# Optimization experiments

Hardware: AMD Instinct MI355X
Metric: run time of the kernel (lower is better)

Reference implementation:

```python
import jax, jax.numpy as jnp
import numpy as np
import math

B, S, D, H = 4, 2048, 1024, 16
HD = D // H  # 64

def setup_inputs() -> dict:
    key = jax.random.key(0)
    ks = jax.random.split(key, 4)
    x = jax.random.normal(ks[0], (B, S, D), dtype=jnp.float32)
    # causal mask, True = attend (precomputed as in the original usage)
    mask = jnp.tril(jnp.ones((S, S), dtype=bool))[None, None, :, :]
    c_attn_w = jax.random.normal(ks[1], (D, 3 * D), dtype=jnp.float32) * 0.02
    c_attn_b = jnp.zeros((3 * D,), dtype=jnp.float32)
    c_proj_w = jax.random.normal(ks[2], (D, D), dtype=jnp.float32) * 0.02
    c_proj_b = jnp.zeros((D,), dtype=jnp.float32)
    return {"x": x, "mask": mask, "c_attn_w": c_attn_w, "c_attn_b": c_attn_b,
            "c_proj_w": c_proj_w, "c_proj_b": c_proj_b}

def reference(x, mask, c_attn_w, c_attn_b, c_proj_w, c_proj_b):
    b, s, d = x.shape
    # c_attn: Conv1D acts as Linear with transposed weight convention
    qkv = x @ c_attn_w + c_attn_b                      # [B,S,3D]
    q, k, v = jnp.split(qkv, 3, axis=-1)
    q = q.reshape(b, s, H, HD).transpose(0, 2, 1, 3)   # [B,H,S,hd]
    k = k.reshape(b, s, H, HD).transpose(0, 2, 1, 3)   # [B,H,S,hd]
    v = v.reshape(b, s, H, HD).transpose(0, 2, 1, 3)   # [B,H,S,hd]
    # scores, scale by sqrt(head_dim) (done unconditionally in _attn)
    w = jnp.einsum('bhqd,bhkd->bhqk', q, k) / math.sqrt(HD)
    # masked_fill_(1 - mask, -10000.0)
    w = jnp.where(mask, w, jnp.float32(-10000.0))
    w = jax.nn.softmax(w, axis=-1)                     # attn_dropout p=0
    a = jnp.einsum('bhqk,bhkd->bhqd', w, v)            # [B,H,S,hd]
    a = a.transpose(0, 2, 1, 3).reshape(b, s, d)       # merge heads
    out = a @ c_proj_w + c_proj_b                      # resid_dropout p=0
    return out
```

## Files before the change

kernel.cpp:

```cpp
#include <hip/hip_runtime.h>

#define SEQ  2048
#define DIM  1024
#define NH   16
#define HD   64
#define NB   4

typedef __bf16 bf16_t;
typedef bf16_t bf16x8 __attribute__((ext_vector_type(8)));
typedef bf16_t bf16x4 __attribute__((ext_vector_type(4)));
typedef float  floatx4 __attribute__((ext_vector_type(4)));

#define MFMA16(a, b, c) __builtin_amdgcn_mfma_f32_16x16x32_bf16((a), (b), (c), 0, 0, 0)

__device__ __forceinline__ void gl_lds16(const bf16_t* g, bf16_t* l) {
    __builtin_amdgcn_global_load_lds(
        (const __attribute__((address_space(1))) void*)g,
        (__attribute__((address_space(3))) void*)l,
        16, 0, 0);
}

__global__ __launch_bounds__(256) void prep(
    const float* __restrict__ x, bf16_t* __restrict__ xb,
    const float* __restrict__ wqkv, bf16_t* __restrict__ wqkvT,
    const float* __restrict__ wproj, bf16_t* __restrict__ wprojT) {
    const int bid = blockIdx.x, tid = threadIdx.x;
    if (bid < 8192) {
        const int i = (bid * 256 + tid) * 4;
        const float4 v = *(const float4*)(x + i);
        xb[i + 0] = (bf16_t)v.x;
        xb[i + 1] = (bf16_t)v.y;
        xb[i + 2] = (bf16_t)v.z;
        xb[i + 3] = (bf16_t)v.w;
        return;
    }
    __shared__ bf16_t t[32][33];
    const float* in;
    bf16_t* out;
    int R, C, bx, by;
    if (bid < 8192 + 3072) {
        const int idx = bid - 8192;
        in = wqkv; out = wqkvT; R = 1024; C = 3072;
        bx = idx % 96; by = idx / 96;
    } else {
        const int idx = bid - 11264;
        in = wproj; out = wprojT; R = 1024; C = 1024;
        bx = idx & 31; by = idx >> 5;
    }
    const int c0 = bx * 32, r0 = by * 32;
    const int tx = tid & 31, ty = tid >> 5;
#pragma unroll
    for (int i = 0; i < 32; i += 8)
        t[ty + i][tx] = (bf16_t)in[(r0 + ty + i) * C + c0 + tx];
    __syncthreads();
#pragma unroll
    for (int i = 0; i < 32; i += 8)
        out[(c0 + ty + i) * R + r0 + tx] = t[tx][ty + i];
}

template <int MODE>
__global__ __launch_bounds__(256, 2) void gemm128(
    const bf16_t* __restrict__ A, const bf16_t* __restrict__ Bt,
    const float* __restrict__ bias, int K,
    bf16_t* __restrict__ Qo, bf16_t* __restrict__ Ko, bf16_t* __restrict__ Vo,
    float* __restrict__ Co) {
    __shared__ __align__(16) bf16_t smem[MODE == 0 ? 128 * 136 : 128 * 128];
    bf16_t* Al = smem;
    bf16_t* Bl = smem + 128 * 64;

    const int tid = threadIdx.x;
    const int m0 = blockIdx.y * 128, n0 = blockIdx.x * 128;
    const int w = tid >> 6, lane = tid & 63;
    const int l15 = lane & 15, quad = lane >> 4;
    const int wm = (w & 1) * 64, wn = (w >> 1) * 64;

    floatx4 acc[4][4] = {};

    const int g_st = ((tid & 7) - (tid >> 3)) & 7;
    const bf16_t* aptr = A + (m0 + (tid >> 3)) * K + g_st * 8;
    const bf16_t* bptr = Bt + (n0 + (tid >> 3)) * K + g_st * 8;
    bf16_t* al = Al + tid * 8;
    bf16_t* bl = Bl + tid * 8;

    for (int k0 = 0; k0 < K; k0 += 64) {
#pragma unroll
        for (int c = 0; c < 4; c++) {
            gl_lds16(aptr + (c * 32) * K, al + c * 2048);
            gl_lds16(bptr + (c * 32) * K, bl + c * 2048);
        }
        aptr += 64;
        bptr += 64;
        __syncthreads();

#pragma unroll
        for (int h = 0; h < 2; h++) {
            const int sAB = (((h << 2) + quad + (l15 & 7)) & 7) * 8;
            bf16x8 af[4], bfr[4];
#pragma unroll
            for (int i = 0; i < 4; i++)
                af[i] = *(const bf16x8*)&Al[(wm + i * 16 + l15) * 64 + sAB];
#pragma unroll
            for (int j = 0; j < 4; j++)
                bfr[j] = *(const bf16x8*)&Bl[(wn + j * 16 + l15) * 64 + sAB];
#pragma unroll
            for (int i = 0; i < 4; i++)
#pragma unroll
                for (int j = 0; j < 4; j++)
                    acc[i][j] = MODE == 0 ? MFMA16(bfr[j], af[i], acc[i][j])
                                          : MFMA16(af[i], bfr[j], acc[i][j]);
        }
        __syncthreads();
    }

    if (MODE == 0) {
        bf16_t* Cl = smem;
        const int which = n0 >> 10;
        const float qs = (which == 0) ? 0.125f * 1.44269504f : 1.0f;
#pragma unroll
        for (int j = 0; j < 4; j++) {
            const int nc = wn + j * 16 + quad * 4;
#pragma unroll
            for (int i = 0; i < 4; i++) {
                const int mrow = wm + i * 16 + l15;
                bf16x4 pk;
#pragma unroll
                for (int r = 0; r < 4; r++)
                    pk[r] = (bf16_t)((acc[i][j][r] + bias[n0 + nc + r]) * qs);
                *(bf16x4*)&Cl[mrow * 136 + nc] = pk;
            }
        }
        __syncthreads();

        if (which < 2) {
            const int row = tid >> 1, ch = (tid & 1) << 6;
            const int m = m0 + row, b = m >> 11, s = m & 2047;
            const int h = ((n0 & 1023) >> 6) + (ch >> 6);
            bf16_t* dst = (which == 0 ? Qo : Ko) + ((size_t)(b * NH + h) * SEQ + s) * HD;
            const bf16_t* src = Cl + row * 136 + ch;
#pragma unroll
            for (int g = 0; g < 8; g++)
                *(bf16x8*)(dst + g * 8) = *(const bf16x8*)(src + g * 8);
        } else {
            const int dl = tid & 127, sh = (tid >> 7) << 6;
            const int h = ((n0 & 1023) >> 6) + (dl >> 6), d = dl & 63;
            const int b = m0 >> 11, sbase = (m0 & 2047) + sh;
            bf16_t* dst = Vo + ((size_t)(b * NH + h) * HD + d) * SEQ + sbase;
#pragma unroll
            for (int g = 0; g < 8; g++) {
                bf16x8 tv;
#pragma unroll
                for (int e = 0; e < 8; e++)
                    tv[e] = Cl[(sh + g * 8 + e) * 136 + dl];
                *(bf16x8*)(dst + g * 8) = tv;
            }
        }
    } else {
#pragma unroll
        for (int j = 0; j < 4; j++) {
            const int n = n0 + wn + j * 16 + l15;
            const float bv = bias[n];
#pragma unroll
            for (int i = 0; i < 4; i++)
#pragma unroll
                for (int r = 0; r < 4; r++) {
                    const int m = m0 + wm + i * 16 + quad * 4 + r;
                    Co[m * 1024 + n] = acc[i][j][r] + bv;
                }
        }
    }
}

__global__ __launch_bounds__(256, 2) void attn2q(
    const bf16_t* __restrict__ Q, const bf16_t* __restrict__ Kg,
    const bf16_t* __restrict__ Vt, bf16_t* __restrict__ Aout) {
    __shared__ bf16_t Ks[2 * 64 * 64];
    __shared__ bf16_t Vs[2 * 64 * 64];
    __shared__ bf16_t Ps[128 * 64];

    const int bh = blockIdx.y;
    const int px = (blockIdx.x + (bh >> 3)) & 7;
    const int qtA = 15 - px, qtB = px;
    const int nkA = 2 * qtA + 2, nkB = 2 * qtB + 2;

    const int tid = threadIdx.x, w = tid >> 6, lane = tid & 63;
    const int l15 = lane & 15, quad = lane >> 4;
    const int b = bh >> 4, hd = bh & 15;
    const int xk = l15 & 7;

    bf16x8 aqA[2][2], aqB[2][2];
#pragma unroll
    for (int i = 0; i < 2; i++) {
        const bf16_t* qrA = Q + (size_t)(bh * SEQ + qtA * 128 + w * 32 + i * 16 + l15) * HD;
        const bf16_t* qrB = Q + (size_t)(bh * SEQ + qtB * 128 + w * 32 + i * 16 + l15) * HD;
#pragma unroll
        for (int h = 0; h < 2; h++) {
            aqA[i][h] = *(const bf16x8*)(qrA + h * 32 + quad * 8);
            aqB[i][h] = *(const bf16x8*)(qrB + h * 32 + quad * 8);
        }
    }

    floatx4 oA[2][4] = {}, oB[2][4] = {};
    float liA[2] = {}, liB[2] = {};

    const int r_st = tid >> 2, g0 = tid & 3;
    const bf16_t* kgl = Kg + (size_t)bh * SEQ * HD + (size_t)r_st * HD;
    const bf16_t* vgl = Vt + (size_t)bh * HD * SEQ + (size_t)r_st * SEQ;
    const int sw0 = ((g0 ^ (r_st & 7)) * 8);
    const int sw1 = (((g0 + 4) ^ (r_st & 7)) * 8);

    auto proc = [&](int qt, bf16x8 (&aq)[2][2], floatx4 (&o)[2][4],
                    float (&li)[2], int kt, int sub) {
        const bf16_t* Ksub = Ks + sub * 4096;
        const bf16_t* Vsub = Vs + sub * 4096;
        bf16x8 bk[4][2];
#pragma unroll
        for (int j = 0; j < 4; j++) {
            const int n = j * 16 + l15;
#pragma unroll
            for (int h = 0; h < 2; h++)
                bk[j][h] = *(const bf16x8*)&Ksub[n * 64 + (((h * 4 + quad) ^ xk) * 8)];
        }
        floatx4 z[2][4] = {};
#pragma unroll
        for (int i = 0; i < 2; i++)
#pragma unroll
            for (int j = 0; j < 4; j++) {
                z[i][j] = MFMA16(bk[j][0], aq[i][0], z[i][j]);
                z[i][j] = MFMA16(bk[j][1], aq[i][1], z[i][j]);
            }
#pragma unroll
        for (int i = 0; i < 2; i++) {
            const int qbase = qt * 128 + w * 32 + i * 16;
            const int qrow_l = qbase + l15;
            const bool full = (kt * 64 + 63) <= qbase;
            const int prow = w * 32 + i * 16 + l15;
            bf16_t* pbase = Ps + prow * 64;
            const int rx = prow & 7;
#pragma unroll
            for (int j = 0; j < 4; j++) {
                const int kg0 = kt * 64 + j * 16 + quad * 4;
                bf16x4 pk;
#pragma unroll
                for (int r = 0; r < 4; r++) {
                    float e = __builtin_amdgcn_exp2f(z[i][j][r]);
                    if (!full && kg0 + r > qrow_l) e = 0.f;
                    li[i] += e;
                    pk[r] = (bf16_t)e;
                }
                const int g = 2 * j + (quad >> 1);
                *(bf16x4*)(pbase + (((g ^ rx) << 3) | ((quad & 1) << 2))) = pk;
            }
        }
        __builtin_amdgcn_s_waitcnt(0xC07F);
        bf16x8 ap[2][2];
#pragma unroll
        for (int i = 0; i < 2; i++) {
            const int row = w * 32 + i * 16 + l15;
#pragma unroll
            for (int kk = 0; kk < 2; kk++)
                ap[i][kk] = *(const bf16x8*)&Ps[row * 64 +
                                               (((kk * 4 + quad) ^ (row & 7)) << 3)];
        }
        bf16x8 bv[4][2];
#pragma unroll
        for (int j = 0; j < 4; j++) {
            const int n = j * 16 + l15;
#pragma unroll
            for (int kk = 0; kk < 2; kk++)
                bv[j][kk] = *(const bf16x8*)&Vsub[n * 64 + (((kk * 4 + quad) ^ xk) * 8)];
        }
#pragma unroll
        for (int i = 0; i < 2; i++)
#pragma unroll
            for (int j = 0; j < 4; j++) {
                o[i][j] = MFMA16(ap[i][0], bv[j][0], o[i][j]);
                o[i][j] = MFMA16(ap[i][1], bv[j][1], o[i][j]);
            }
    };

    for (int ktp = 0; ktp < nkA; ktp += 2) {
#pragma unroll
        for (int sub = 0; sub < 2; ++sub) {
            const int kt = ktp + sub;
            const bf16x8 k0 = *(const bf16x8*)(kgl + kt * 64 * HD + g0 * 8);
            const bf16x8 k1 = *(const bf16x8*)(kgl + kt * 64 * HD + (g0 + 4) * 8);
            const bf16x8 v0 = *(const bf16x8*)(vgl + kt * 64 + g0 * 8);
            const bf16x8 v1 = *(const bf16x8*)(vgl + kt * 64 + (g0 + 4) * 8);
            bf16_t* ks = Ks + sub * 4096 + r_st * 64;
            bf16_t* vs = Vs + sub * 4096 + r_st * 64;
            *(bf16x8*)(ks + sw0) = k0;
            *(bf16x8*)(ks + sw1) = k1;
            *(bf16x8*)(vs + sw0) = v0;
            *(bf16x8*)(vs + sw1) = v1;
        }
        __syncthreads();
#pragma unroll
        for (int sub = 0; sub < 2; ++sub) {
            const int kt = ktp + sub;
            proc(qtA, aqA, oA, liA, kt, sub);
            if (kt < nkB) proc(qtB, aqB, oB, liB, kt, sub);
        }
        __syncthreads();
    }

#pragma unroll
    for (int t = 0; t < 2; t++) {
        const int qt = t == 0 ? qtA : qtB;
        floatx4(&o)[2][4] = t == 0 ? oA : oB;
        float(&li)[2] = t == 0 ? liA : liB;
#pragma unroll
        for (int i = 0; i < 2; i++) {
            float s = li[i];
            s += __shfl_xor(s, 16, 64);
            s += __shfl_xor(s, 32, 64);
#pragma unroll
            for (int r = 0; r < 4; r++) {
                const float sv = __shfl(s, quad * 4 + r, 64);
                const float inv = 1.0f / sv;
                const int srow = qt * 128 + w * 32 + i * 16 + quad * 4 + r;
                bf16_t* orow = Aout + (size_t)(b * SEQ + srow) * DIM + hd * HD;
#pragma unroll
                for (int j = 0; j < 4; j++)
                    orow[j * 16 + l15] = (bf16_t)(o[i][j][r] * inv);
            }
        }
    }
}

extern "C" void kernel_launch(void* const* d_in, const int* in_sizes, int n_in,
                              void* d_out, int out_size, void* d_ws, size_t ws_size,
                              hipStream_t stream) {
    const float* x        = (const float*)d_in[0];
    const float* c_attn_w = (const float*)d_in[2];
    const float* c_attn_b = (const float*)d_in[3];
    const float* c_proj_w = (const float*)d_in[4];
    const float* c_proj_b = (const float*)d_in[5];
    float* out = (float*)d_out;

    char* ws = (char*)d_ws;
    bf16_t* xb     = (bf16_t*)ws; ws += (size_t)NB * SEQ * DIM * 2;
    bf16_t* wqkvT  = (bf16_t*)ws; ws += (size_t)3072 * 1024 * 2;
    bf16_t* wprojT = (bf16_t*)ws; ws += (size_t)1024 * 1024 * 2;
    bf16_t* Qb  = (bf16_t*)ws; ws += (size_t)NB * NH * SEQ * HD * 2;
    bf16_t* Kb  = (bf16_t*)ws; ws += (size_t)NB * NH * SEQ * HD * 2;
    bf16_t* Vtb = (bf16_t*)ws; ws += (size_t)NB * NH * SEQ * HD * 2;
    bf16_t* Ab  = (bf16_t*)ws; ws += (size_t)NB * SEQ * DIM * 2;

    prep<<<12288, 256, 0, stream>>>(x, xb, c_attn_w, wqkvT, c_proj_w, wprojT);

    gemm128<0><<<dim3(24, 64), 256, 0, stream>>>(xb, wqkvT, c_attn_b, 1024,
                                                 Qb, Kb, Vtb, nullptr);

    attn2q<<<dim3(8, NB * NH), 256, 0, stream>>>(Qb, Kb, Vtb, Ab);

    gemm128<1><<<dim3(8, 64), 256, 0, stream>>>(Ab, wprojT, c_proj_b, 1024,
                                                nullptr, nullptr, nullptr, out);
}
```

Baseline: 267.0 us.

## Prefetch next K/V tile pair into registers during attention compute

The attention loop now issues the global loads for the next pair of K/V tiles into registers before computing the current pair. Only the LDS stores are waited on before the barrier, so those global loads stay in flight while the MFMAs run instead of stalling each iteration. The row-sum accumulator is also split into four independent partial sums per row, which shortens the serial add chain after each exp; the partials are combined at the end. The cost is extra registers for the prefetch buffers, which may lower occupancy.

```diff
diff --git a/kernel.cpp b/kernel.cpp
--- a/kernel.cpp
+++ b/kernel.cpp
@@ -200,7 +200,7 @@
     }
 
     floatx4 oA[2][4] = {}, oB[2][4] = {};
-    float liA[2] = {}, liB[2] = {};
+    floatx4 liA[2] = {}, liB[2] = {};
 
     const int r_st = tid >> 2, g0 = tid & 3;
     const bf16_t* kgl = Kg + (size_t)bh * SEQ * HD + (size_t)r_st * HD;
@@ -208,8 +208,20 @@
     const int sw0 = ((g0 ^ (r_st & 7)) * 8);
     const int sw1 = (((g0 + 4) ^ (r_st & 7)) * 8);
 
+    bf16x8 rk0[2], rk1[2], rv0[2], rv1[2];
+    auto gload = [&](int ktp) {
+#pragma unroll
+        for (int sub = 0; sub < 2; ++sub) {
+            const int kt = ktp + sub;
+            rk0[sub] = *(const bf16x8*)(kgl + kt * 64 * HD + g0 * 8);
+            rk1[sub] = *(const bf16x8*)(kgl + kt * 64 * HD + (g0 + 4) * 8);
+            rv0[sub] = *(const bf16x8*)(vgl + kt * 64 + g0 * 8);
+            rv1[sub] = *(const bf16x8*)(vgl + kt * 64 + (g0 + 4) * 8);
+        }
+    };
+
     auto proc = [&](int qt, bf16x8 (&aq)[2][2], floatx4 (&o)[2][4],
-                    float (&li)[2], int kt, int sub) {
+                    floatx4 (&li)[2], int kt, int sub) {
         const bf16_t* Ksub = Ks + sub * 4096;
         const bf16_t* Vsub = Vs + sub * 4096;
         bf16x8 bk[4][2];
@@ -244,7 +256,7 @@
                 for (int r = 0; r < 4; r++) {
                     float e = __builtin_amdgcn_exp2f(z[i][j][r]);
                     if (!full && kg0 + r > qrow_l) e = 0.f;
-                    li[i] += e;
+                    li[i][r] += e;
                     pk[r] = (bf16_t)e;
                 }
                 const int g = 2 * j + (quad >> 1);
@@ -278,39 +290,37 @@
             }
     };
 
+    gload(0);
     for (int ktp = 0; ktp < nkA; ktp += 2) {
 #pragma unroll
         for (int sub = 0; sub < 2; ++sub) {
-            const int kt = ktp + sub;
-            const bf16x8 k0 = *(const bf16x8*)(kgl + kt * 64 * HD + g0 * 8);
-            const bf16x8 k1 = *(const bf16x8*)(kgl + kt * 64 * HD + (g0 + 4) * 8);
-            const bf16x8 v0 = *(const bf16x8*)(vgl + kt * 64 + g0 * 8);
-            const bf16x8 v1 = *(const bf16x8*)(vgl + kt * 64 + (g0 + 4) * 8);
             bf16_t* ks = Ks + sub * 4096 + r_st * 64;
             bf16_t* vs = Vs + sub * 4096 + r_st * 64;
-            *(bf16x8*)(ks + sw0) = k0;
-            *(bf16x8*)(ks + sw1) = k1;
-            *(bf16x8*)(vs + sw0) = v0;
-            *(bf16x8*)(vs + sw1) = v1;
-        }
-        __syncthreads();
+            *(bf16x8*)(ks + sw0) = rk0[sub];
+            *(bf16x8*)(ks + sw1) = rk1[sub];
+            *(bf16x8*)(vs + sw0) = rv0[sub];
+            *(bf16x8*)(vs + sw1) = rv1[sub];
+        }
+        if (ktp + 2 < nkA) gload(ktp + 2);
+        __builtin_amdgcn_s_waitcnt(0xC07F);
+        __builtin_amdgcn_s_barrier();
 #pragma unroll
         for (int sub = 0; sub < 2; ++sub) {
             const int kt = ktp + sub;
             proc(qtA, aqA, oA, liA, kt, sub);
             if (kt < nkB) proc(qtB, aqB, oB, liB, kt, sub);
         }
-        __syncthreads();
+        __builtin_amdgcn_s_barrier();
     }
 
 #pragma unroll
     for (int t = 0; t < 2; t++) {
         const int qt = t == 0 ? qtA : qtB;
         floatx4(&o)[2][4] = t == 0 ? oA : oB;
-        float(&li)[2] = t == 0 ? liA : liB;
+        floatx4(&li)[2] = t == 0 ? liA : liB;
 #pragma unroll
         for (int i = 0; i < 2; i++) {
-            float s = li[i];
+            float s = li[i][0] + li[i][1] + li[i][2] + li[i][3];
             s += __shfl_xor(s, 16, 64);
             s += __shfl_xor(s, 32, 64);
 #pragma unroll
```

Result: slower. 361.3 us (+35.3%).
